# Optimization experiments

Measured on AMD Instinct MI355X. Metric: run time of the kernel, lower is better.

## Reference

```python
import jax, jax.numpy as jnp
import numpy as np

B, N_IN, N_OUT = 16, 7000, 28000
C_IN, C_OUT, S = 64, 64, 9
NNZ = 3 * N_OUT  # ~3 source verts per upsampled vert (barycentric)


def setup_inputs() -> dict:
    key = jax.random.key(0)
    k = jax.random.split(key, 6)
    x = jax.random.normal(k[0], (B, N_IN, C_IN), dtype=jnp.float32)
    values = jax.random.uniform(k[1], (NNZ,), dtype=jnp.float32)
    row = jax.random.randint(k[2], (NNZ,), 0, N_OUT)
    col = jax.random.randint(k[3], (NNZ,), 0, N_IN)
    spiral_indices = jax.random.randint(k[4], (N_OUT, S), 0, N_OUT)
    weight = jax.random.normal(k[5], (S * C_IN, C_OUT), dtype=jnp.float32) * 0.02
    bias = jnp.zeros((C_OUT,), dtype=jnp.float32)
    return {"x": x, "values": values, "weight": weight, "bias": bias,
            "row": row, "col": col, "spiral_indices": spiral_indices}


def reference(x, values, weight, bias, row, col, spiral_indices):
    # Pool: gather source verts, scale by sparse matrix values, scatter-add to output verts
    n_out = spiral_indices.shape[0]
    gathered = x[:, col, :] * values[None, :, None]            # [B, nnz, C]
    pooled = jnp.zeros((x.shape[0], n_out, x.shape[2]), x.dtype).at[:, row, :].add(gathered)  # [B, N_out, C]
    # SpiralConv: gather spiral neighborhood, flatten, linear
    feat = pooled[:, spiral_indices.reshape(-1), :]            # [B, N_out*S, C]
    feat = feat.reshape(x.shape[0], n_out, -1)                 # [B, N_out, S*C]
    out = jax.nn.elu(jnp.einsum('bnf,fo->bno', feat, weight) + bias)
    return out
```

## Files before the change

### kernel.cpp

```cpp
#include <hip/hip_runtime.h>
#include <math.h>

#define B      16
#define N_IN   7000
#define N_OUT  28000
#define C      64
#define S      9
#define NNZ    (3 * N_OUT)
#define F      (S * C)
#define KB     (F / 32)

#define MT     110

typedef short bf16x8 __attribute__((ext_vector_type(8)));
typedef float f32x4  __attribute__((ext_vector_type(4)));

static __device__ __forceinline__ unsigned short f2bf(float f) {
    unsigned u = __float_as_uint(f);
    u += 0x7fffu + ((u >> 16) & 1u);
    return (unsigned short)(u >> 16);
}

__global__ void hist_kernel(const int* __restrict__ row, int* __restrict__ cnt) {
    int i = blockIdx.x * 256 + threadIdx.x;
    if (i < NNZ) atomicAdd(&cnt[row[i]], 1);
}

__global__ void scan_kernel(const int* __restrict__ cnt,
                            int* __restrict__ offs, int* __restrict__ cursor) {
    __shared__ int tmp[1024];
    const int t = threadIdx.x;
    const int base = t * 28;
    const bool live = (t < 1000);

    int c[28];
    int partial = 0;
    if (live) {
        #pragma unroll
        for (int j = 0; j < 28; ++j) { c[j] = cnt[base + j]; partial += c[j]; }
    }
    tmp[t] = partial;
    __syncthreads();
    #pragma unroll
    for (int off = 1; off < 1024; off <<= 1) {
        int v = (t >= off) ? tmp[t - off] : 0;
        __syncthreads();
        tmp[t] += v;
        __syncthreads();
    }
    if (live) {
        int run = tmp[t] - partial;
        #pragma unroll
        for (int j = 0; j < 28; ++j) {
            offs[base + j]   = run;
            cursor[base + j] = run;
            run += c[j];
        }
        if (t == 999) offs[N_OUT] = run;
    }
}

__global__ void place_kernel(const int* __restrict__ row, const int* __restrict__ col,
                             const float* __restrict__ values,
                             int* __restrict__ cursor,
                             int* __restrict__ ecol, float* __restrict__ eval) {
    int i = blockIdx.x * 256 + threadIdx.x;
    if (i < NNZ) {
        int pos = atomicAdd(&cursor[row[i]], 1);
        ecol[pos] = col[i];
        eval[pos] = values[i];
    }
}

__global__ void xt_kernel(const float* __restrict__ x, float* __restrict__ xT) {
    const int n  = blockIdx.x;
    const int t  = threadIdx.x;
    const int b  = t >> 4;
    const int ch = (t & 15) * 4;
    const float4 v = *(const float4*)(x + ((size_t)b * N_IN + n) * C + ch);
    *(float4*)(xT + ((size_t)n * B + b) * C + ch) = v;
}

__global__ void pool_kernel(const float* __restrict__ xT,
                            const int*   __restrict__ ecol,
                            const float* __restrict__ eval,
                            const int*   __restrict__ offs,
                            unsigned short* __restrict__ pooled) {
    const int wave = threadIdx.x >> 6;
    const int lane = threadIdx.x & 63;
    const int r    = blockIdx.x * 4 + wave;

    const int start = offs[r], end = offs[r + 1];

    float4 acc[4];
    #pragma unroll
    for (int j = 0; j < 4; ++j) acc[j] = make_float4(0.f, 0.f, 0.f, 0.f);

    for (int e = start; e < end; ++e) {
        const int   cl = ecol[e];
        const float v  = eval[e];
        const float* base = xT + (size_t)cl * (B * C) + lane * 4;
        float4 xv[4];
        #pragma unroll
        for (int j = 0; j < 4; ++j)
            xv[j] = *(const float4*)(base + j * 256);
        #pragma unroll
        for (int j = 0; j < 4; ++j) {
            acc[j].x = fmaf(xv[j].x, v, acc[j].x);
            acc[j].y = fmaf(xv[j].y, v, acc[j].y);
            acc[j].z = fmaf(xv[j].z, v, acc[j].z);
            acc[j].w = fmaf(xv[j].w, v, acc[j].w);
        }
    }

    unsigned short* dst = pooled + (size_t)r * (B * C) + lane * 4;
    #pragma unroll
    for (int j = 0; j < 4; ++j) {
        unsigned long long ov =
            (unsigned long long)f2bf(acc[j].x)
            | ((unsigned long long)f2bf(acc[j].y) << 16)
            | ((unsigned long long)f2bf(acc[j].z) << 32)
            | ((unsigned long long)f2bf(acc[j].w) << 48);
        __builtin_nontemporal_store(ov, (unsigned long long*)(dst + j * 256));
    }
}

__global__ void packw_kernel(const float* __restrict__ w, unsigned short* __restrict__ pw) {
    const int kb   = blockIdx.x;
    const int nt   = threadIdx.x >> 6;
    const int lane = threadIdx.x & 63;
    const int lm   = lane & 15;
    const int quad = lane >> 4;

    unsigned short v[8];
    #pragma unroll
    for (int j = 0; j < 8; ++j) {
        const int k = kb * 32 + quad * 8 + j;
        const int n = nt * 16 + lm;
        v[j] = f2bf(w[(size_t)k * C + n]);
    }
    unsigned short* dst = pw + ((size_t)(kb * 4 + nt) * 64 + lane) * 8;
    #pragma unroll
    for (int j = 0; j < 8; ++j) dst[j] = v[j];
}

__global__ __launch_bounds__(512, 4)
void spiral_mfma(const unsigned short* __restrict__ pooled,
                 const bf16x8*         __restrict__ packedW,
                 const int*            __restrict__ sp,
                 const float*          __restrict__ bias,
                 float*                __restrict__ out) {
    const int L = blockIdx.x;
    int b, mtile;
    if (L < 8 * MT) { b = L & 7;                  mtile = L >> 3; }
    else            { b = 8 + ((L - 8 * MT) & 7); mtile = (L - 8 * MT) >> 3; }

    const int wave = threadIdx.x >> 6;
    const int lane = threadIdx.x & 63;
    const int lm   = lane & 15;
    const int quad = lane >> 4;
    const int m_base = mtile * 256 + wave * 32;

    __shared__ bf16x8 bw[KB * 4 * 64];
    {
        const int t = threadIdx.x;
        #pragma unroll
        for (int i = 0; i < 9; ++i)
            bw[i * 512 + t] = packedW[i * 512 + t];
    }

    int spv[S];
    {
        int r = m_base + (lane & 31);
        if (r >= N_OUT) r = N_OUT - 1;
        #pragma unroll
        for (int s = 0; s < S; ++s) spv[s] = sp[r * S + s];
    }

    const unsigned short* poolb = pooled + (size_t)b * C;

    f32x4 acc[2][4];
    #pragma unroll
    for (int t = 0; t < 2; ++t)
        #pragma unroll
        for (int nt = 0; nt < 4; ++nt)
            acc[t][nt] = (f32x4){0.f, 0.f, 0.f, 0.f};

    int    rowi[2][2];
    bf16x8 abuf[2][2][2];

    #pragma unroll
    for (int t = 0; t < 2; ++t)
        rowi[0][t] = __shfl(spv[0], t * 16 + lm, 64);
    #pragma unroll
    for (int half = 0; half < 2; ++half) {
        const int c0 = half * 32 + quad * 8;
        #pragma unroll
        for (int t = 0; t < 2; ++t)
            abuf[0][half][t] =
                *(const bf16x8*)(poolb + (size_t)rowi[0][t] * (B * C) + c0);
    }

    __syncthreads();

    #pragma unroll
    for (int s = 0; s < S; ++s) {
        const int cur = s & 1, nxt = cur ^ 1;

        if (s + 1 < S) {
            #pragma unroll
            for (int t = 0; t < 2; ++t)
                rowi[nxt][t] = __shfl(spv[s + 1], t * 16 + lm, 64);
            #pragma unroll
            for (int half = 0; half < 2; ++half) {
                const int c0 = half * 32 + quad * 8;
                #pragma unroll
                for (int t = 0; t < 2; ++t)
                    abuf[nxt][half][t] =
                        *(const bf16x8*)(poolb + (size_t)rowi[nxt][t] * (B * C) + c0);
            }
        }

        #pragma unroll
        for (int half = 0; half < 2; ++half) {
            bf16x8 bb[4];
            #pragma unroll
            for (int nt = 0; nt < 4; ++nt)
                bb[nt] = bw[((s * 2 + half) * 4 + nt) * 64 + lane];
            #pragma unroll
            for (int nt = 0; nt < 4; ++nt)
                #pragma unroll
                for (int t = 0; t < 2; ++t)
                    acc[t][nt] = __builtin_amdgcn_mfma_f32_16x16x32_bf16(
                        abuf[cur][half][t], bb[nt], acc[t][nt], 0, 0, 0);
        }
    }

    #pragma unroll
    for (int nt = 0; nt < 4; ++nt) {
        const int n = nt * 16 + lm;
        const float bs = bias[n];
        #pragma unroll
        for (int t = 0; t < 2; ++t) {
            #pragma unroll
            for (int reg = 0; reg < 4; ++reg) {
                const int r = m_base + t * 16 + quad * 4 + reg;
                if (r < N_OUT) {
                    float v = acc[t][nt][reg] + bs;
                    v = v > 0.f ? v : (__expf(v) - 1.0f);
                    __builtin_nontemporal_store(v,
                        out + ((size_t)b * N_OUT + r) * C + n);
                }
            }
        }
    }
}

extern "C" void kernel_launch(void* const* d_in, const int* in_sizes, int n_in,
                              void* d_out, int out_size, void* d_ws, size_t ws_size,
                              hipStream_t stream) {
    const float* x      = (const float*)d_in[0];
    const float* values = (const float*)d_in[1];
    const float* weight = (const float*)d_in[2];
    const float* bias   = (const float*)d_in[3];
    const int*   row    = (const int*)d_in[4];
    const int*   col    = (const int*)d_in[5];
    const int*   sp     = (const int*)d_in[6];
    float*       out    = (float*)d_out;

    char* ws = (char*)d_ws;
    size_t off = 0;
    unsigned short* pooled  = (unsigned short*)(ws + off); off += (size_t)N_OUT * B * C * 2;
    unsigned short* packedW = (unsigned short*)(ws + off); off += (size_t)KB * 4 * 64 * 8 * 2;
    float* xT     = (float*)(ws + off); off += (size_t)N_IN * B * C * 4;
    int*   offs   = (int*)(ws + off); off += ((size_t)(N_OUT + 1) * 4 + 124) / 128 * 128;
    int*   cursor = (int*)(ws + off); off += (size_t)N_OUT * 4 + 128;
    int*   cnt    = (int*)(ws + off); off += (size_t)N_OUT * 4 + 128;
    int*   ecol   = (int*)(ws + off); off += (size_t)NNZ * 4;
    float* eval   = (float*)(ws + off); off += (size_t)NNZ * 4;

    (void)hipMemsetAsync(cnt, 0, (size_t)N_OUT * 4, stream);
    hist_kernel <<<(NNZ + 255) / 256, 256, 0, stream>>>(row, cnt);
    scan_kernel <<<1, 1024, 0, stream>>>(cnt, offs, cursor);
    place_kernel<<<(NNZ + 255) / 256, 256, 0, stream>>>(row, col, values, cursor, ecol, eval);

    packw_kernel<<<KB, 256, 0, stream>>>(weight, packedW);

    xt_kernel<<<N_IN, 256, 0, stream>>>(x, xT);

    pool_kernel<<<N_OUT / 4, 256, 0, stream>>>(xT, ecol, eval, offs, pooled);

    spiral_mfma<<<B * MT, 512, 0, stream>>>(pooled,
        reinterpret_cast<const bf16x8*>(packedW), sp, bias, out);
}
```

Before: 343.9 us.

## Share spiral row gathers across batches via LDS staging in spiral MFMA

The pooled buffer becomes two batch groups of eight, with each vertex row holding 512 contiguous bf16 values (8 batches × 64 channels). Each spiral block now covers 32 output vertices for 8 batches, one batch per wave. Whole 1 KB rows are gathered cooperatively into XOR-swizzled LDS, so each spiral index is fetched once per group rather than once per batch. The cost is an extra LDS round trip, a barrier on every spiral step, and launch bounds relaxed to 2 blocks per SM because of the added shared memory.

```diff
diff --git a/kernel.cpp b/kernel.cpp
--- a/kernel.cpp
+++ b/kernel.cpp
@@ -9,8 +9,6 @@
 #define NNZ    (3 * N_OUT)
 #define F      (S * C)
 #define KB     (F / 32)
-
-#define MT     110
 
 typedef short bf16x8 __attribute__((ext_vector_type(8)));
 typedef float f32x4  __attribute__((ext_vector_type(4)));
@@ -113,15 +111,18 @@
         }
     }
 
-    unsigned short* dst = pooled + (size_t)r * (B * C) + lane * 4;
     #pragma unroll
     for (int j = 0; j < 4; ++j) {
+        const int g  = j >> 1;
+        const int bp = (j & 1) * 4 + (lane >> 4);
         unsigned long long ov =
             (unsigned long long)f2bf(acc[j].x)
             | ((unsigned long long)f2bf(acc[j].y) << 16)
             | ((unsigned long long)f2bf(acc[j].z) << 32)
             | ((unsigned long long)f2bf(acc[j].w) << 48);
-        __builtin_nontemporal_store(ov, (unsigned long long*)(dst + j * 256));
+        unsigned short* dst = pooled + (size_t)g * (N_OUT * 512)
+                            + (size_t)r * 512 + bp * 64 + (lane & 15) * 4;
+        __builtin_nontemporal_store(ov, (unsigned long long*)dst);
     }
 }
 
@@ -144,24 +145,25 @@
     for (int j = 0; j < 8; ++j) dst[j] = v[j];
 }
 
-__global__ __launch_bounds__(512, 4)
+__global__ __launch_bounds__(512, 2)
 void spiral_mfma(const unsigned short* __restrict__ pooled,
                  const bf16x8*         __restrict__ packedW,
                  const int*            __restrict__ sp,
                  const float*          __restrict__ bias,
                  float*                __restrict__ out) {
-    const int L = blockIdx.x;
-    int b, mtile;
-    if (L < 8 * MT) { b = L & 7;                  mtile = L >> 3; }
-    else            { b = 8 + ((L - 8 * MT) & 7); mtile = (L - 8 * MT) >> 3; }
-
-    const int wave = threadIdx.x >> 6;
-    const int lane = threadIdx.x & 63;
-    const int lm   = lane & 15;
-    const int quad = lane >> 4;
-    const int m_base = mtile * 256 + wave * 32;
-
-    __shared__ bf16x8 bw[KB * 4 * 64];
+    const int Lb    = blockIdx.x;
+    const int g     = Lb & 1;
+    const int mtile = Lb >> 1;
+    const int wave  = threadIdx.x >> 6;
+    const int lane  = threadIdx.x & 63;
+    const int lm    = lane & 15;
+    const int quad  = lane >> 4;
+    const int m_base = mtile * 32;
+    const int b      = g * 8 + wave;
+
+    __shared__ bf16x8         bw[KB * 4 * 64];
+    __shared__ unsigned short apool[2][32][512];
+
     {
         const int t = threadIdx.x;
         #pragma unroll
@@ -171,13 +173,12 @@
 
     int spv[S];
     {
-        int r = m_base + (lane & 31);
-        if (r >= N_OUT) r = N_OUT - 1;
+        const int r = m_base + (lane & 31);
         #pragma unroll
         for (int s = 0; s < S; ++s) spv[s] = sp[r * S + s];
     }
 
-    const unsigned short* poolb = pooled + (size_t)b * C;
+    const unsigned short* pgbase = pooled + (size_t)g * (N_OUT * 512);
 
     f32x4 acc[2][4];
     #pragma unroll
@@ -186,21 +187,18 @@
         for (int nt = 0; nt < 4; ++nt)
             acc[t][nt] = (f32x4){0.f, 0.f, 0.f, 0.f};
 
-    int    rowi[2][2];
-    bf16x8 abuf[2][2][2];
-
-    #pragma unroll
-    for (int t = 0; t < 2; ++t)
-        rowi[0][t] = __shfl(spv[0], t * 16 + lm, 64);
-    #pragma unroll
-    for (int half = 0; half < 2; ++half) {
-        const int c0 = half * 32 + quad * 8;
-        #pragma unroll
-        for (int t = 0; t < 2; ++t)
-            abuf[0][half][t] =
-                *(const bf16x8*)(poolb + (size_t)rowi[0][t] * (B * C) + c0);
-    }
-
+    bf16x8 ld[4];
+
+    #pragma unroll
+    for (int q = 0; q < 4; ++q) {
+        const int r = __shfl(spv[0], wave * 4 + q, 64);
+        ld[q] = *(const bf16x8*)(pgbase + (size_t)r * 512 + lane * 8);
+    }
+    #pragma unroll
+    for (int q = 0; q < 4; ++q) {
+        const int j = wave * 4 + q;
+        *(bf16x8*)(&apool[0][j][(lane ^ (j & 7)) * 8]) = ld[q];
+    }
     __syncthreads();
 
     #pragma unroll
@@ -209,15 +207,9 @@
 
         if (s + 1 < S) {
             #pragma unroll
-            for (int t = 0; t < 2; ++t)
-                rowi[nxt][t] = __shfl(spv[s + 1], t * 16 + lm, 64);
-            #pragma unroll
-            for (int half = 0; half < 2; ++half) {
-                const int c0 = half * 32 + quad * 8;
-                #pragma unroll
-                for (int t = 0; t < 2; ++t)
-                    abuf[nxt][half][t] =
-                        *(const bf16x8*)(poolb + (size_t)rowi[nxt][t] * (B * C) + c0);
+            for (int q = 0; q < 4; ++q) {
+                const int r = __shfl(spv[s + 1], wave * 4 + q, 64);
+                ld[q] = *(const bf16x8*)(pgbase + (size_t)r * 512 + lane * 8);
             }
         }
 
@@ -227,13 +219,29 @@
             #pragma unroll
             for (int nt = 0; nt < 4; ++nt)
                 bb[nt] = bw[((s * 2 + half) * 4 + nt) * 64 + lane];
+            bf16x8 aa[2];
+            #pragma unroll
+            for (int t = 0; t < 2; ++t) {
+                const int j = t * 16 + lm;
+                const int chunk = wave * 8 + (((half * 4 + quad) ^ (j & 7)));
+                aa[t] = *(const bf16x8*)(&apool[cur][j][chunk * 8]);
+            }
             #pragma unroll
             for (int nt = 0; nt < 4; ++nt)
                 #pragma unroll
                 for (int t = 0; t < 2; ++t)
                     acc[t][nt] = __builtin_amdgcn_mfma_f32_16x16x32_bf16(
-                        abuf[cur][half][t], bb[nt], acc[t][nt], 0, 0, 0);
-        }
+                        aa[t], bb[nt], acc[t][nt], 0, 0, 0);
+        }
+
+        if (s + 1 < S) {
+            #pragma unroll
+            for (int q = 0; q < 4; ++q) {
+                const int j = wave * 4 + q;
+                *(bf16x8*)(&apool[nxt][j][(lane ^ (j & 7)) * 8]) = ld[q];
+            }
+        }
+        __syncthreads();
     }
 
     #pragma unroll
@@ -245,12 +253,10 @@
             #pragma unroll
             for (int reg = 0; reg < 4; ++reg) {
                 const int r = m_base + t * 16 + quad * 4 + reg;
-                if (r < N_OUT) {
-                    float v = acc[t][nt][reg] + bs;
-                    v = v > 0.f ? v : (__expf(v) - 1.0f);
-                    __builtin_nontemporal_store(v,
-                        out + ((size_t)b * N_OUT + r) * C + n);
-                }
+                float v = acc[t][nt][reg] + bs;
+                v = v > 0.f ? v : (__expf(v) - 1.0f);
+                __builtin_nontemporal_store(v,
+                    out + ((size_t)b * N_OUT + r) * C + n);
             }
         }
     }
@@ -270,7 +276,7 @@
 
     char* ws = (char*)d_ws;
     size_t off = 0;
-    unsigned short* pooled  = (unsigned short*)(ws + off); off += (size_t)N_OUT * B * C * 2;
+    unsigned short* pooled  = (unsigned short*)(ws + off); off += (size_t)B * N_OUT * C * 2;
     unsigned short* packedW = (unsigned short*)(ws + off); off += (size_t)KB * 4 * 64 * 8 * 2;
     float* xT     = (float*)(ws + off); off += (size_t)N_IN * B * C * 4;
     int*   offs   = (int*)(ws + off); off += ((size_t)(N_OUT + 1) * 4 + 124) / 128 * 128;
@@ -290,6 +296,6 @@
 
     pool_kernel<<<N_OUT / 4, 256, 0, stream>>>(xT, ecol, eval, offs, pooled);
 
-    spiral_mfma<<<B * MT, 512, 0, stream>>>(pooled,
+    spiral_mfma<<<875 * 2, 512, 0, stream>>>(pooled,
         reinterpret_cast<const bf16x8*>(packedW), sp, bias, out);
 }
```

After: 321.0 us. 1.07x faster.
